# Kernel tuning notes

Measured on AMD Instinct MI355X. Metric: run time of the kernel, lower is better.

Reference implementation:

```python
import jax, jax.numpy as jnp
import numpy as np

B, N_DET, N_T, NY, NX = 4, 128, 2048, 256, 256


def setup_inputs() -> dict:
    key = jax.random.key(0)
    k1, k2, k3 = jax.random.split(key, 3)
    sino = jax.random.normal(k1, (B, 1, N_DET, N_T), dtype=jnp.float32)
    # LUT channel 0: floor temporal index (stored as float, cast to int in forward)
    k_floor = jax.random.randint(k2, (NY, NX, N_DET), 0, N_T).astype(jnp.float32)
    # LUT channel 1: linear interpolation weight alpha in [0,1)
    alpha = jax.random.uniform(k3, (NY, NX, N_DET), dtype=jnp.float32)
    lut = jnp.stack([k_floor, alpha], axis=-1)  # [NY, NX, N_DET, 2]
    return {"sino": sino, "lut": lut}


def reference(sino, lut):
    # sino: [B, 1, n_det, n_t]; lut: [ny, nx, n_det, 2]
    b, c, n_det, n_t = sino.shape
    k_floor = lut[..., 0].astype(jnp.int32)          # [ny, nx, n_det]
    alpha = lut[..., 1]                               # [ny, nx, n_det]
    valid = (k_floor >= 0) & (k_floor < n_t - 1)
    k0 = jnp.clip(k_floor, 0, n_t - 2)
    k1 = k0 + 1
    S = sino[:, 0]                                    # [B, n_det, n_t]
    det = jnp.arange(n_det)                           # broadcasts against [ny,nx,n_det]
    s0 = S[:, det, k0]                                # [B, ny, nx, n_det]
    s1 = S[:, det, k1]                                # [B, ny, nx, n_det]
    sk = (1.0 - alpha) * s0 + alpha * s1
    sk = jnp.where(valid, sk, jnp.zeros_like(sk))
    # Hann apodization window over detectors
    apod = (0.5 - 0.5 * jnp.cos(2.0 * jnp.pi * jnp.arange(n_det, dtype=jnp.float32)
                                / max(n_det - 1, 1))).astype(sino.dtype)
    out = jnp.einsum('bijd,d->bij', sk, apod)
    norm = jnp.maximum(apod.sum(), 1e-06)
    out = out / norm
    return out[:, None]                               # [B, 1, ny, nx]
```

## Files before the change

kernel.cpp:

```cpp
#include <hip/hip_runtime.h>
#include <hip/hip_fp16.h>


#define NB      4
#define NDET    128
#define NT      2048
#define NPIX    65536
#define DBLOCK  8
#define DQ      4
#define PTILE   2048
#define THREADS 1024
#define PXPT    (PTILE / THREADS)

__global__ __launch_bounds__(256)
void cvt_kernel(const float* __restrict__ sino, uint2* __restrict__ ws16) {
    const int id = blockIdx.x * 256 + threadIdx.x;
    float v0 = sino[id];
    float v1 = sino[id + NDET * NT];
    float v2 = sino[id + 2 * NDET * NT];
    float v3 = sino[id + 3 * NDET * NT];
    __half2 h01 = __floats2half2_rn(v0, v1);
    __half2 h23 = __floats2half2_rn(v2, v3);
    uint2 u;
    u.x = *(const unsigned*)&h01;
    u.y = *(const unsigned*)&h23;
    ws16[id] = u;
}

__global__ __launch_bounds__(THREADS, 4)
void bp_kernel(const uint2* __restrict__ ws16,
               const float* __restrict__ lut,
               float* __restrict__ out) {
    __shared__ uint2 lds2[DQ * NT];

    const int tid   = threadIdx.x;
    const int octet = blockIdx.x & 15;
    const int tile  = blockIdx.x >> 4;
    const int d0    = octet * DBLOCK;
    const int px0   = tile * PTILE;

    float apod[DBLOCK];
#pragma unroll
    for (int j = 0; j < DBLOCK; ++j) {
        float x = (float)(d0 + j) * (6.28318530717958647692f / 127.0f);
        apod[j] = 0.5f - 0.5f * __cosf(x);
    }

    float acc[PXPT][NB];
#pragma unroll
    for (int i = 0; i < PXPT; ++i)
#pragma unroll
        for (int b = 0; b < NB; ++b) acc[i][b] = 0.0f;

    const float4* lp[PXPT];
#pragma unroll
    for (int i = 0; i < PXPT; ++i)
        lp[i] = (const float4*)
            (lut + ((size_t)(px0 + tid + i * THREADS) * NDET + d0) * 2);

    float4 Lcur[PXPT][2];
#pragma unroll
    for (int i = 0; i < PXPT; ++i) {
        Lcur[i][0] = lp[i][0];
        Lcur[i][1] = lp[i][1];
    }

    {
        const uint4* src = (const uint4*)(ws16 + (size_t)d0 * NT);
        uint4* dst = (uint4*)lds2;
#pragma unroll
        for (int r = 0; r < 4; ++r) dst[tid + r * THREADS] = src[tid + r * THREADS];
    }
    __syncthreads();

    float4 Lnext[PXPT][2];
#pragma unroll
    for (int i = 0; i < PXPT; ++i) {
        Lnext[i][0] = lp[i][2];
        Lnext[i][1] = lp[i][3];
    }

    auto gather = [&](const float4 (*Lq)[2], int jbase) {
#pragma unroll
        for (int i = 0; i < PXPT; ++i) {
#pragma unroll
            for (int q = 0; q < 2; ++q) {
                float4 Le = Lq[i][q];
#pragma unroll
                for (int h = 0; h < 2; ++h) {
                    float kf = h ? Le.z : Le.x;
                    float af = h ? Le.w : Le.y;
                    int   dl = q * 2 + h;
                    int k = (int)kf;
                    bool valid = (unsigned)k < (unsigned)(NT - 1);
                    float w  = valid ? apod[jbase + dl] : 0.0f;
                    int  k0  = valid ? k : 0;
                    uint2 e0 = lds2[dl * NT + k0];
                    uint2 e1 = lds2[dl * NT + k0 + 1];
                    __half2 a01 = *(__half2*)&e0.x, a23 = *(__half2*)&e0.y;
                    __half2 b01 = *(__half2*)&e1.x, b23 = *(__half2*)&e1.y;
                    __half2 a2  = __float2half2_rn(af);
                    __half2 s01 = __hfma2(a2, __hsub2(b01, a01), a01);
                    __half2 s23 = __hfma2(a2, __hsub2(b23, a23), a23);
                    float2 f01 = __half22float2(s01);
                    float2 f23 = __half22float2(s23);
                    acc[i][0] = fmaf(w, f01.x, acc[i][0]);
                    acc[i][1] = fmaf(w, f01.y, acc[i][1]);
                    acc[i][2] = fmaf(w, f23.x, acc[i][2]);
                    acc[i][3] = fmaf(w, f23.y, acc[i][3]);
                }
            }
        }
    };

    gather(Lcur, 0);
    __syncthreads();

    {
        const uint4* src = (const uint4*)(ws16 + (size_t)(d0 + DQ) * NT);
        uint4* dst = (uint4*)lds2;
#pragma unroll
        for (int r = 0; r < 4; ++r) dst[tid + r * THREADS] = src[tid + r * THREADS];
    }
    __syncthreads();

    gather(Lnext, DQ);

    const float inv_norm = 1.0f / 63.5f;
#pragma unroll
    for (int i = 0; i < PXPT; ++i) {
        const int px = px0 + tid + i * THREADS;
#pragma unroll
        for (int b = 0; b < NB; ++b) {
            atomicAdd(&out[(size_t)b * NPIX + px], acc[i][b] * inv_norm);
        }
    }
}

__global__ __launch_bounds__(512, 4)
void bp_fallback(const float* __restrict__ sino,
                 const float* __restrict__ lut,
                 float* __restrict__ out) {
    __shared__ __half2 lds[4][NT];
    const int tid   = threadIdx.x;
    const int octet = blockIdx.x & 15;
    const int tile  = blockIdx.x >> 4;
    const int d0    = octet * DBLOCK;
    const int px0   = tile * 1024;
    float apod[DBLOCK];
#pragma unroll
    for (int j = 0; j < DBLOCK; ++j) {
        float x = (float)(d0 + j) * (6.28318530717958647692f / 127.0f);
        apod[j] = 0.5f - 0.5f * __cosf(x);
    }
    float4 L[2][4];
#pragma unroll
    for (int i = 0; i < 2; ++i) {
        const float4* lq = (const float4*)
            (lut + ((size_t)(px0 + tid + i * 512) * NDET + d0) * 2);
#pragma unroll
        for (int q = 0; q < 4; ++q) L[i][q] = lq[q];
    }
    float acc[2][NB];
#pragma unroll
    for (int i = 0; i < 2; ++i)
#pragma unroll
        for (int b = 0; b < NB; ++b) acc[i][b] = 0.0f;
    const float4* s4 = (const float4*)sino;
    for (int ph = 0; ph < 4; ++ph) {
        const int b0  = (ph >> 1) * 2;
        const int dh  = ph & 1;
        const int dg0 = d0 + dh * 4;
        if (ph) __syncthreads();
        for (int f = tid; f < 4 * (NT / 4); f += 512) {
            int dl = f >> 9;
            int t4 = f & 511;
            size_t row = ((size_t)b0 * NDET + dg0 + dl) * (NT / 4) + t4;
            float4 ve = s4[row];
            float4 vo = s4[row + (size_t)NDET * (NT / 4)];
            __half2* dstp = &lds[dl][t4 * 4];
            dstp[0] = __floats2half2_rn(ve.x, vo.x);
            dstp[1] = __floats2half2_rn(ve.y, vo.y);
            dstp[2] = __floats2half2_rn(ve.z, vo.z);
            dstp[3] = __floats2half2_rn(ve.w, vo.w);
        }
        __syncthreads();
#pragma unroll
        for (int i = 0; i < 2; ++i) {
#pragma unroll
            for (int q2 = 0; q2 < 2; ++q2) {
                float4 Lq = L[i][dh * 2 + q2];
#pragma unroll
                for (int h = 0; h < 2; ++h) {
                    float kf = h ? Lq.z : Lq.x;
                    float af = h ? Lq.w : Lq.y;
                    int   dl = q2 * 2 + h;
                    int k = (int)kf;
                    bool valid = (unsigned)k < (unsigned)(NT - 1);
                    float w  = valid ? apod[dh * 4 + dl] : 0.0f;
                    int  k0  = valid ? k : 0;
                    __half2 s0v = lds[dl][k0];
                    __half2 s1v = lds[dl][k0 + 1];
                    __half2 a2  = __float2half2_rn(af);
                    __half2 sk  = __hfma2(a2, __hsub2(s1v, s0v), s0v);
                    float2  fv  = __half22float2(sk);
                    acc[i][b0 + 0] = fmaf(w, fv.x, acc[i][b0 + 0]);
                    acc[i][b0 + 1] = fmaf(w, fv.y, acc[i][b0 + 1]);
                }
            }
        }
    }
    const float inv_norm = 1.0f / 63.5f;
#pragma unroll
    for (int i = 0; i < 2; ++i) {
        const int px = px0 + tid + i * 512;
#pragma unroll
        for (int b = 0; b < NB; ++b)
            atomicAdd(&out[(size_t)b * NPIX + px], acc[i][b] * inv_norm);
    }
}

extern "C" void kernel_launch(void* const* d_in, const int* in_sizes, int n_in,
                              void* d_out, int out_size, void* d_ws, size_t ws_size,
                              hipStream_t stream) {
    const float* sino = (const float*)d_in[0];
    const float* lut  = (const float*)d_in[1];
    float* out = (float*)d_out;

    (void)hipMemsetAsync(d_out, 0, (size_t)out_size * sizeof(float), stream);

    const size_t ws_needed = (size_t)NDET * NT * sizeof(uint2);
    if (ws_size >= ws_needed) {
        uint2* ws16 = (uint2*)d_ws;
        cvt_kernel<<<dim3(NDET * NT / 256), dim3(256), 0, stream>>>(sino, ws16);
        bp_kernel<<<dim3(512), dim3(THREADS), 0, stream>>>(ws16, lut, out);
    } else {
        bp_fallback<<<dim3(1024), dim3(512), 0, stream>>>(sino, lut, out);
    }
}
```

Baseline: 126.4 us.

## Gather interpolation pairs from global memory with wave-per-pixel detector reduction

Adds a conversion kernel that packs each sample with its successor as 16-byte fp16 entries, so one global load fetches both interpolation endpoints for all four batches. A new backprojection kernel maps each wave's 64 lanes to 128 detectors for a small group of pixels, reads the LUT with coalesced nontemporal loads, and reduces across lanes with DPP. Results are written directly, which removes the output memset, the atomics and the LDS staging. The cost is a workspace twice as large, random gathers served from L2 instead of LDS, and a cross-lane reduction for every pixel and batch.

```diff
diff --git a/kernel.cpp b/kernel.cpp
--- a/kernel.cpp
+++ b/kernel.cpp
@@ -6,6 +6,108 @@
 #define NDET    128
 #define NT      2048
 #define NPIX    65536
+#define PXW     8
+
+typedef unsigned uv4 __attribute__((ext_vector_type(4)));
+
+__global__ __launch_bounds__(256)
+void cvt16b(const float* __restrict__ sino, uint4* __restrict__ ws) {
+    const int id = blockIdx.x * 256 + threadIdx.x;
+    const int t  = id & (NT - 1);
+    float c0 = sino[id];
+    float c1 = sino[id +     NDET * NT];
+    float c2 = sino[id + 2 * NDET * NT];
+    float c3 = sino[id + 3 * NDET * NT];
+    const int idn = (t < NT - 1) ? id + 1 : id;
+    float n0 = sino[idn];
+    float n1 = sino[idn +     NDET * NT];
+    float n2 = sino[idn + 2 * NDET * NT];
+    float n3 = sino[idn + 3 * NDET * NT];
+    uint4 u;
+    __half2 h;
+    h = __floats2half2_rn(c0, c1); u.x = *(unsigned*)&h;
+    h = __floats2half2_rn(c2, c3); u.y = *(unsigned*)&h;
+    h = __floats2half2_rn(n0, n1); u.z = *(unsigned*)&h;
+    h = __floats2half2_rn(n2, n3); u.w = *(unsigned*)&h;
+    ws[id] = u;
+}
+
+__device__ __forceinline__ float wave_reduce_add(float v) {
+    int x;
+    x = __builtin_amdgcn_update_dpp(0, __float_as_int(v), 0xB1,  0xF, 0xF, true); v += __int_as_float(x);
+    x = __builtin_amdgcn_update_dpp(0, __float_as_int(v), 0x4E,  0xF, 0xF, true); v += __int_as_float(x);
+    x = __builtin_amdgcn_update_dpp(0, __float_as_int(v), 0x141, 0xF, 0xF, true); v += __int_as_float(x);
+    x = __builtin_amdgcn_update_dpp(0, __float_as_int(v), 0x140, 0xF, 0xF, true); v += __int_as_float(x);
+    x = __builtin_amdgcn_update_dpp(0, __float_as_int(v), 0x142, 0xF, 0xF, true); v += __int_as_float(x);
+    x = __builtin_amdgcn_update_dpp(0, __float_as_int(v), 0x143, 0xF, 0xF, true); v += __int_as_float(x);
+    return v;
+}
+
+__device__ __forceinline__ void lerp_acc(unsigned kbits, unsigned abits,
+                                         const uint4* __restrict__ row,
+                                         float apod_d, float acc[NB]) {
+    int k = (int)__uint_as_float(kbits);
+    bool valid = (unsigned)k < (unsigned)(NT - 1);
+    int k0 = valid ? k : 0;
+    uint4 e = row[k0];
+    float af = __uint_as_float(abits);
+    __half2 a01 = *(__half2*)&e.x, a23 = *(__half2*)&e.y;
+    __half2 b01 = *(__half2*)&e.z, b23 = *(__half2*)&e.w;
+    __half2 a2  = __float2half2_rn(af);
+    __half2 s01 = __hfma2(a2, __hsub2(b01, a01), a01);
+    __half2 s23 = __hfma2(a2, __hsub2(b23, a23), a23);
+    float w = valid ? apod_d : 0.0f;
+    float2 f01 = __half22float2(s01);
+    float2 f23 = __half22float2(s23);
+    acc[0] = fmaf(w, f01.x, acc[0]);
+    acc[1] = fmaf(w, f01.y, acc[1]);
+    acc[2] = fmaf(w, f23.x, acc[2]);
+    acc[3] = fmaf(w, f23.y, acc[3]);
+}
+
+__global__ __launch_bounds__(256, 4)
+void bp_det(const uint4* __restrict__ ws,
+            const float* __restrict__ lut,
+            float* __restrict__ out) {
+    const int tid  = threadIdx.x;
+    const int lane = tid & 63;
+    const int wid  = (blockIdx.x << 2) + (tid >> 6);
+    const int px0  = wid * PXW;
+
+    const int d0 = 2 * lane, d1 = 2 * lane + 1;
+    const float C = 6.28318530717958647692f / 127.0f;
+    const float apod0 = 0.5f - 0.5f * __cosf((float)d0 * C);
+    const float apod1 = 0.5f - 0.5f * __cosf((float)d1 * C);
+
+    const uint4* row0 = ws + (size_t)d0 * NT;
+    const uint4* row1 = ws + (size_t)d1 * NT;
+    const uv4*  lut4  = (const uv4*)lut;
+
+    float res[NB] = {0.f, 0.f, 0.f, 0.f};
+
+#pragma unroll
+    for (int j = 0; j < PXW; ++j) {
+        const int px = px0 + j;
+        uv4 l = __builtin_nontemporal_load(lut4 + ((size_t)px * 64 + lane));
+        float acc[NB] = {0.f, 0.f, 0.f, 0.f};
+        lerp_acc(l.x, l.y, row0, apod0, acc);
+        lerp_acc(l.z, l.w, row1, apod1, acc);
+#pragma unroll
+        for (int b = 0; b < NB; ++b) {
+            float t = wave_reduce_add(acc[b]);
+            float t63 = __shfl(t, 63, 64);
+            res[b] = (lane == j) ? t63 : res[b];
+        }
+    }
+
+    const float inv_norm = 1.0f / 63.5f;
+    if (lane < PXW) {
+#pragma unroll
+        for (int b = 0; b < NB; ++b)
+            out[(size_t)b * NPIX + px0 + lane] = res[b] * inv_norm;
+    }
+}
+
 #define DBLOCK  8
 #define DQ      4
 #define PTILE   2048
@@ -227,14 +329,20 @@
     const float* lut  = (const float*)d_in[1];
     float* out = (float*)d_out;
 
-    (void)hipMemsetAsync(d_out, 0, (size_t)out_size * sizeof(float), stream);
-
-    const size_t ws_needed = (size_t)NDET * NT * sizeof(uint2);
-    if (ws_size >= ws_needed) {
+    const size_t ws_new = (size_t)NDET * NT * sizeof(uint4);
+    const size_t ws_old = (size_t)NDET * NT * sizeof(uint2);
+
+    if (ws_size >= ws_new) {
+        uint4* ws = (uint4*)d_ws;
+        cvt16b<<<dim3(NDET * NT / 256), dim3(256), 0, stream>>>(sino, ws);
+        bp_det<<<dim3(NPIX / PXW / 4), dim3(256), 0, stream>>>(ws, lut, out);
+    } else if (ws_size >= ws_old) {
+        (void)hipMemsetAsync(d_out, 0, (size_t)out_size * sizeof(float), stream);
         uint2* ws16 = (uint2*)d_ws;
         cvt_kernel<<<dim3(NDET * NT / 256), dim3(256), 0, stream>>>(sino, ws16);
         bp_kernel<<<dim3(512), dim3(THREADS), 0, stream>>>(ws16, lut, out);
     } else {
+        (void)hipMemsetAsync(d_out, 0, (size_t)out_size * sizeof(float), stream);
         bp_fallback<<<dim3(1024), dim3(512), 0, stream>>>(sino, lut, out);
     }
 }
```

Result: slower. 144.7 us (+14.5%).

## Stage full detector octet in LDS and software-pipeline nontemporal LUT loads

Applied to the files above, without the earlier changes.

The backprojection kernel now loads all 8 detector rows for its octet into shared memory at once (128 KB), removing the mid-kernel resync and second staging phase. Each thread handles 4 pixels with a double-buffered, manually waited (s_waitcnt) pipeline of nontemporal LUT loads, and the grid halves to 256 blocks. Larger LDS use limits blocks per CU and may reduce occupancy and latency hiding. The fewer, larger blocks may also leave CUs idle on a 256-CU device.

```diff
diff --git a/kernel.cpp b/kernel.cpp
--- a/kernel.cpp
+++ b/kernel.cpp
@@ -6,11 +6,12 @@
 #define NDET    128
 #define NT      2048
 #define NPIX    65536
-#define DBLOCK  8
-#define DQ      4
-#define PTILE   2048
-#define THREADS 1024
-#define PXPT    (PTILE / THREADS)
+#define OCT     8
+#define PTILE   4096
+#define THR     1024
+#define PXT     (PTILE / THR)
+
+typedef float fv4 __attribute__((ext_vector_type(4)));
 
 __global__ __launch_bounds__(256)
 void cvt_kernel(const float* __restrict__ sino, uint2* __restrict__ ws16) {
@@ -27,113 +28,102 @@
     ws16[id] = u;
 }
 
-__global__ __launch_bounds__(THREADS, 4)
-void bp_kernel(const uint2* __restrict__ ws16,
-               const float* __restrict__ lut,
-               float* __restrict__ out) {
-    __shared__ uint2 lds2[DQ * NT];
+__global__ __launch_bounds__(THR, 4)
+void bp_oct(const uint2* __restrict__ ws16,
+            const float* __restrict__ lut,
+            float* __restrict__ out) {
+    __shared__ uint2 lds[OCT * NT];
 
     const int tid   = threadIdx.x;
-    const int octet = blockIdx.x & 15;
-    const int tile  = blockIdx.x >> 4;
-    const int d0    = octet * DBLOCK;
+    const int octet = blockIdx.x >> 4;
+    const int tile  = blockIdx.x & 15;
+    const int d0    = octet * OCT;
     const int px0   = tile * PTILE;
 
-    float apod[DBLOCK];
-#pragma unroll
-    for (int j = 0; j < DBLOCK; ++j) {
+    float apod[OCT];
+#pragma unroll
+    for (int j = 0; j < OCT; ++j) {
         float x = (float)(d0 + j) * (6.28318530717958647692f / 127.0f);
         apod[j] = 0.5f - 0.5f * __cosf(x);
     }
 
-    float acc[PXPT][NB];
-#pragma unroll
-    for (int i = 0; i < PXPT; ++i)
-#pragma unroll
-        for (int b = 0; b < NB; ++b) acc[i][b] = 0.0f;
-
-    const float4* lp[PXPT];
-#pragma unroll
-    for (int i = 0; i < PXPT; ++i)
-        lp[i] = (const float4*)
-            (lut + ((size_t)(px0 + tid + i * THREADS) * NDET + d0) * 2);
-
-    float4 Lcur[PXPT][2];
-#pragma unroll
-    for (int i = 0; i < PXPT; ++i) {
-        Lcur[i][0] = lp[i][0];
-        Lcur[i][1] = lp[i][1];
-    }
-
     {
         const uint4* src = (const uint4*)(ws16 + (size_t)d0 * NT);
-        uint4* dst = (uint4*)lds2;
-#pragma unroll
-        for (int r = 0; r < 4; ++r) dst[tid + r * THREADS] = src[tid + r * THREADS];
+        uint4* dst = (uint4*)lds;
+#pragma unroll
+        for (int r = 0; r < 8; ++r) dst[tid + r * THR] = src[tid + r * THR];
     }
     __syncthreads();
 
-    float4 Lnext[PXPT][2];
-#pragma unroll
-    for (int i = 0; i < PXPT; ++i) {
-        Lnext[i][0] = lp[i][2];
-        Lnext[i][1] = lp[i][3];
-    }
-
-    auto gather = [&](const float4 (*Lq)[2], int jbase) {
-#pragma unroll
-        for (int i = 0; i < PXPT; ++i) {
-#pragma unroll
-            for (int q = 0; q < 2; ++q) {
-                float4 Le = Lq[i][q];
-#pragma unroll
-                for (int h = 0; h < 2; ++h) {
-                    float kf = h ? Le.z : Le.x;
-                    float af = h ? Le.w : Le.y;
-                    int   dl = q * 2 + h;
-                    int k = (int)kf;
-                    bool valid = (unsigned)k < (unsigned)(NT - 1);
-                    float w  = valid ? apod[jbase + dl] : 0.0f;
-                    int  k0  = valid ? k : 0;
-                    uint2 e0 = lds2[dl * NT + k0];
-                    uint2 e1 = lds2[dl * NT + k0 + 1];
-                    __half2 a01 = *(__half2*)&e0.x, a23 = *(__half2*)&e0.y;
-                    __half2 b01 = *(__half2*)&e1.x, b23 = *(__half2*)&e1.y;
-                    __half2 a2  = __float2half2_rn(af);
-                    __half2 s01 = __hfma2(a2, __hsub2(b01, a01), a01);
-                    __half2 s23 = __hfma2(a2, __hsub2(b23, a23), a23);
-                    float2 f01 = __half22float2(s01);
-                    float2 f23 = __half22float2(s23);
-                    acc[i][0] = fmaf(w, f01.x, acc[i][0]);
-                    acc[i][1] = fmaf(w, f01.y, acc[i][1]);
-                    acc[i][2] = fmaf(w, f23.x, acc[i][2]);
-                    acc[i][3] = fmaf(w, f23.y, acc[i][3]);
-                }
+    const fv4* lbase = (const fv4*)lut
+                     + (size_t)(px0 + tid) * (NDET / 2) + octet * 4;
+
+    float acc[PXT][NB];
+#pragma unroll
+    for (int i = 0; i < PXT; ++i)
+#pragma unroll
+        for (int b = 0; b < NB; ++b) acc[i][b] = 0.0f;
+
+    fv4 lv[2][4];
+#pragma unroll
+    for (int q = 0; q < 4; ++q)
+        lv[0][q] = __builtin_nontemporal_load(lbase + q);
+#pragma unroll
+    for (int q = 0; q < 4; ++q)
+        lv[1][q] = __builtin_nontemporal_load(lbase + 65536 + q);
+
+#pragma unroll
+    for (int i = 0; i < PXT; ++i) {
+        if (i + 1 < PXT) {
+            asm volatile("s_waitcnt vmcnt(4)" ::: "memory");
+        } else {
+            asm volatile("s_waitcnt vmcnt(0)" ::: "memory");
+        }
+        __builtin_amdgcn_sched_barrier(0);
+
+#pragma unroll
+        for (int q = 0; q < 4; ++q) {
+            const fv4 Le = lv[i & 1][q];
+#pragma unroll
+            for (int h = 0; h < 2; ++h) {
+                const int dl = 2 * q + h;
+                float kf = h ? Le.z : Le.x;
+                float af = h ? Le.w : Le.y;
+                int   k  = (int)kf;
+                bool  valid = (unsigned)k < (unsigned)(NT - 1);
+                int   k0 = valid ? k : 0;
+                float w  = valid ? apod[dl] : 0.0f;
+                uint2 e0 = lds[dl * NT + k0];
+                uint2 e1 = lds[dl * NT + k0 + 1];
+                __half2 a01 = *(__half2*)&e0.x, a23 = *(__half2*)&e0.y;
+                __half2 b01 = *(__half2*)&e1.x, b23 = *(__half2*)&e1.y;
+                __half2 a2  = __float2half2_rn(af);
+                __half2 s01 = __hfma2(a2, __hsub2(b01, a01), a01);
+                __half2 s23 = __hfma2(a2, __hsub2(b23, a23), a23);
+                float2 f01 = __half22float2(s01);
+                float2 f23 = __half22float2(s23);
+                acc[i][0] = fmaf(w, f01.x, acc[i][0]);
+                acc[i][1] = fmaf(w, f01.y, acc[i][1]);
+                acc[i][2] = fmaf(w, f23.x, acc[i][2]);
+                acc[i][3] = fmaf(w, f23.y, acc[i][3]);
             }
         }
-    };
-
-    gather(Lcur, 0);
-    __syncthreads();
-
-    {
-        const uint4* src = (const uint4*)(ws16 + (size_t)(d0 + DQ) * NT);
-        uint4* dst = (uint4*)lds2;
-#pragma unroll
-        for (int r = 0; r < 4; ++r) dst[tid + r * THREADS] = src[tid + r * THREADS];
-    }
-    __syncthreads();
-
-    gather(Lnext, DQ);
+
+        if (i + 2 < PXT) {
+#pragma unroll
+            for (int q = 0; q < 4; ++q)
+                lv[i & 1][q] = __builtin_nontemporal_load(
+                    lbase + (size_t)(i + 2) * 65536 + q);
+        }
+    }
 
     const float inv_norm = 1.0f / 63.5f;
 #pragma unroll
-    for (int i = 0; i < PXPT; ++i) {
-        const int px = px0 + tid + i * THREADS;
-#pragma unroll
-        for (int b = 0; b < NB; ++b) {
+    for (int i = 0; i < PXT; ++i) {
+        const int px = px0 + tid + i * THR;
+#pragma unroll
+        for (int b = 0; b < NB; ++b)
             atomicAdd(&out[(size_t)b * NPIX + px], acc[i][b] * inv_norm);
-        }
     }
 }
 
@@ -145,11 +135,11 @@
     const int tid   = threadIdx.x;
     const int octet = blockIdx.x & 15;
     const int tile  = blockIdx.x >> 4;
-    const int d0    = octet * DBLOCK;
+    const int d0    = octet * 8;
     const int px0   = tile * 1024;
-    float apod[DBLOCK];
-#pragma unroll
-    for (int j = 0; j < DBLOCK; ++j) {
+    float apod[8];
+#pragma unroll
+    for (int j = 0; j < 8; ++j) {
         float x = (float)(d0 + j) * (6.28318530717958647692f / 127.0f);
         apod[j] = 0.5f - 0.5f * __cosf(x);
     }
@@ -233,7 +223,7 @@
     if (ws_size >= ws_needed) {
         uint2* ws16 = (uint2*)d_ws;
         cvt_kernel<<<dim3(NDET * NT / 256), dim3(256), 0, stream>>>(sino, ws16);
-        bp_kernel<<<dim3(512), dim3(THREADS), 0, stream>>>(ws16, lut, out);
+        bp_oct<<<dim3(256), dim3(THR), 0, stream>>>(ws16, lut, out);
     } else {
         bp_fallback<<<dim3(1024), dim3(512), 0, stream>>>(sino, lut, out);
     }
```

New measurement: 173.0 us. 1.37x slower.
